# Kernel tuning notes

Measured on AMD Instinct MI355X. Metric: run time of the kernel, lower is better.

## Reference

```python
import jax, jax.numpy as jnp
import numpy as np


def _cubic(x):
    absx = np.abs(x)
    absx2 = absx ** 2
    absx3 = absx ** 3
    return ((1.5 * absx3 - 2.5 * absx2 + 1) * (absx <= 1)
            + (-0.5 * absx3 + 2.5 * absx2 - 4 * absx + 2) * ((1 < absx) & (absx <= 2)))


def _contributions(in_length, out_length, scale):
    # Replicates Resizer.contributions for cubic kernel with antialiasing (scale < 1).
    kernel_width = 4.0 / scale
    fixed_kernel = lambda arg: scale * _cubic(scale * arg)
    out_coordinates = np.arange(1, out_length + 1)
    shifted = out_coordinates - (out_length - in_length * scale) / 2
    match = shifted / scale + 0.5 * (1 - 1 / scale)
    left = np.floor(match - kernel_width / 2)
    expanded = int(np.ceil(kernel_width) + 2)
    fov = np.int16(left[:, None] + np.arange(expanded) - 1)  # (out, taps)
    weights = fixed_kernel(1.0 * match[:, None] - fov - 1)
    s = np.sum(weights, axis=1)
    s[s == 0] = 1.0
    weights = weights / s[:, None]
    mirror = np.concatenate((np.arange(in_length), np.arange(in_length - 1, -1, -1)))
    fov = mirror[np.mod(fov, mirror.shape[0])]
    nz = np.nonzero(np.any(weights, axis=0))[0]  # drop all-zero taps
    return weights[:, nz], fov[:, nz]


IN_SHAPE = (32, 3, 512, 512)
OUT_HW = 256
SCALE = 0.5
NDIM_TRAIL = 3  # len(scale_factor) - 1 trailing singleton dims on weights


def setup_inputs() -> dict:
    key = jax.random.key(0)
    in_tensor = jax.random.normal(key, IN_SHAPE, dtype=jnp.float32)
    w_np, fov_np = _contributions(IN_SHAPE[2], OUT_HW, SCALE)
    taps, out_len = w_np.shape[1], w_np.shape[0]
    w = jnp.asarray(w_np.T.reshape((taps, out_len) + (1,) * NDIM_TRAIL), dtype=jnp.float32)
    fov = jnp.asarray(fov_np.T, dtype=jnp.int32)  # (taps, out)
    # H and W have identical in/out lengths and scale -> identical tables
    return {"in_tensor": in_tensor, "w2": w, "fov2": fov, "w3": w, "fov3": fov}


def reference(in_tensor, w2, fov2, w3, fov3):
    x = in_tensor
    for dim, fov, w in ((2, fov2, w2), (3, fov3, w3)):
        x = jnp.swapaxes(x, dim, 0)          # bring resized axis to front
        x = jnp.sum(x[fov] * w, axis=0)      # gather (taps,out,...) * w -> (out,...)
        x = jnp.swapaxes(x, dim, 0)
    return x
```

## Files before the change

kernel.cpp:

```cpp
#include <hip/hip_runtime.h>


#define H_IN   512
#define W_IN   512
#define H_OUT  256
#define W_OUT  256
#define BC     96
#define TAPS   8
#define OH_T   8
#define OW_T   128
#define IN_ROWS (2 * OH_T + 6)
#define MID_COLS (2 * OW_T + 6)

__device__ __forceinline__ int mir(int r, int n) {
    r = (r < 0) ? (-1 - r) : r;
    r = (r >= n) ? (2 * n - 1 - r) : r;
    return r;
}

__global__ __launch_bounds__(256) void resize_fused(const float* __restrict__ in,
                                                    const float* __restrict__ wt,
                                                    float* __restrict__ out) {
    __shared__ float mid[OH_T][MID_COLS];

    const int bid = blockIdx.x;
    const int owt = bid & 1;
    const int oht = (bid >> 1) & 31;
    const int bc  = bid >> 6;
    const int oh0 = oht * OH_T;
    const int ow0 = owt * OW_T;
    const int t   = threadIdx.x;

    float K[TAPS];
#pragma unroll
    for (int i = 0; i < TAPS; ++i) K[i] = wt[i * H_OUT];

    const float* src = in + (size_t)bc * H_IN * W_IN;
    const int rbase = 2 * oh0 - 3;
    const int cbase = 2 * ow0 - 3;

    for (int c = t; c < MID_COLS; c += 256) {
        const int gc = mir(cbase + c, W_IN);
        float acc[OH_T];
#pragma unroll
        for (int k = 0; k < OH_T; ++k) acc[k] = 0.f;

#pragma unroll
        for (int r = 0; r < IN_ROWS; ++r) {
            const float x = src[(size_t)mir(rbase + r, H_IN) * W_IN + gc];
#pragma unroll
            for (int k = 0; k < OH_T; ++k) {
                const int i = r - 2 * k;
                if (0 <= i && i < TAPS) acc[k] += K[i] * x;
            }
        }
#pragma unroll
        for (int k = 0; k < OH_T; ++k) mid[k][c] = acc[k];
    }

    __syncthreads();

    const int owl = t & (OW_T - 1);
    const int r0  = (t >> 7) * 4;
    float* dst = out + ((size_t)bc * H_OUT + oh0) * W_OUT + ow0 + owl;

#pragma unroll
    for (int rr = 0; rr < 4; ++rr) {
        const int row = r0 + rr;
        float s = 0.f;
#pragma unroll
        for (int j = 0; j < TAPS; ++j)
            s += K[j] * mid[row][2 * owl + j];
        dst[(size_t)row * W_OUT] = s;
    }
}

extern "C" void kernel_launch(void* const* d_in, const int* in_sizes, int n_in,
                              void* d_out, int out_size, void* d_ws, size_t ws_size,
                              hipStream_t stream) {
    const float* in = (const float*)d_in[0];
    const float* w2 = (const float*)d_in[1];
    float* out = (float*)d_out;
    (void)d_ws; (void)ws_size;

    resize_fused<<<BC * 32 * 2, 256, 0, stream>>>(in, w2, out);
}
```

Baseline: 158.5 us.

## Process full-width row tiles with float4 loads and register-windowed horizontal pass

Each block now covers a full 512-column input strip for 8 output rows instead of splitting width into two tiles. This removes the duplicated halo columns and column mirroring in the vertical pass. The vertical pass uses float4 global loads per thread. The horizontal pass builds a 24-element register window from shared memory, computes 8 outputs per thread, and stores them as float4, handling mirroring only at the edge column groups. Blocks shrink to 128 threads and the grid is halved, which may reduce occupancy and latency hiding. The W-dimension weights are now read from their own input instead of reusing the H table.

```diff
diff --git a/kernel.cpp b/kernel.cpp
--- a/kernel.cpp
+++ b/kernel.cpp
@@ -8,9 +8,8 @@
 #define BC     96
 #define TAPS   8
 #define OH_T   8
-#define OW_T   128
 #define IN_ROWS (2 * OH_T + 6)
-#define MID_COLS (2 * OW_T + 6)
+#define MID_STRIDE 514
 
 __device__ __forceinline__ int mir(int r, int n) {
     r = (r < 0) ? (-1 - r) : r;
@@ -18,60 +17,90 @@
     return r;
 }
 
-__global__ __launch_bounds__(256) void resize_fused(const float* __restrict__ in,
-                                                    const float* __restrict__ wt,
+__global__ __launch_bounds__(128) void resize_fused(const float* __restrict__ in,
+                                                    const float* __restrict__ wh,
+                                                    const float* __restrict__ ww,
                                                     float* __restrict__ out) {
-    __shared__ float mid[OH_T][MID_COLS];
+    __shared__ float mid[OH_T * MID_STRIDE];
 
-    const int bid = blockIdx.x;
-    const int owt = bid & 1;
-    const int oht = (bid >> 1) & 31;
-    const int bc  = bid >> 6;
-    const int oh0 = oht * OH_T;
-    const int ow0 = owt * OW_T;
+    const int oht = blockIdx.x & 31;
+    const int bc  = blockIdx.x >> 5;
     const int t   = threadIdx.x;
 
-    float K[TAPS];
+    float KH[TAPS];
 #pragma unroll
-    for (int i = 0; i < TAPS; ++i) K[i] = wt[i * H_OUT];
+    for (int i = 0; i < TAPS; ++i) KH[i] = wh[i * H_OUT];
 
-    const float* src = in + (size_t)bc * H_IN * W_IN;
-    const int rbase = 2 * oh0 - 3;
-    const int cbase = 2 * ow0 - 3;
+    const float4* src = (const float4*)(in + (size_t)bc * H_IN * W_IN) + t;
+    const int rbase = 16 * oht - 3;
 
-    for (int c = t; c < MID_COLS; c += 256) {
-        const int gc = mir(cbase + c, W_IN);
-        float acc[OH_T];
+    float4 acc[OH_T];
 #pragma unroll
-        for (int k = 0; k < OH_T; ++k) acc[k] = 0.f;
+    for (int k = 0; k < OH_T; ++k) acc[k] = make_float4(0.f, 0.f, 0.f, 0.f);
 
 #pragma unroll
-        for (int r = 0; r < IN_ROWS; ++r) {
-            const float x = src[(size_t)mir(rbase + r, H_IN) * W_IN + gc];
+    for (int r = 0; r < IN_ROWS; ++r) {
+        const int rm = mir(rbase + r, H_IN);
+        const float4 x = src[(size_t)rm * (W_IN / 4)];
 #pragma unroll
-            for (int k = 0; k < OH_T; ++k) {
-                const int i = r - 2 * k;
-                if (0 <= i && i < TAPS) acc[k] += K[i] * x;
+        for (int k = 0; k < OH_T; ++k) {
+            const int i = r - 2 * k;
+            if (0 <= i && i < TAPS) {
+                const float kw = KH[i];
+                acc[k].x += kw * x.x;
+                acc[k].y += kw * x.y;
+                acc[k].z += kw * x.z;
+                acc[k].w += kw * x.w;
             }
         }
+    }
 #pragma unroll
-        for (int k = 0; k < OH_T; ++k) mid[k][c] = acc[k];
+    for (int k = 0; k < OH_T; ++k) {
+        float2* m2 = (float2*)&mid[k * MID_STRIDE + 4 * t];
+        m2[0] = make_float2(acc[k].x, acc[k].y);
+        m2[1] = make_float2(acc[k].z, acc[k].w);
     }
 
     __syncthreads();
 
-    const int owl = t & (OW_T - 1);
-    const int r0  = (t >> 7) * 4;
-    float* dst = out + ((size_t)bc * H_OUT + oh0) * W_OUT + ow0 + owl;
+    float KW[TAPS];
+#pragma unroll
+    for (int i = 0; i < TAPS; ++i) KW[i] = ww[i * W_OUT];
+
+    const int r   = t & 7;
+    const int cg0 = t >> 3;
+    const int oh  = 8 * oht + r;
+    float* drow = out + ((size_t)bc * H_OUT + oh) * W_OUT;
 
 #pragma unroll
-    for (int rr = 0; rr < 4; ++rr) {
-        const int row = r0 + rr;
-        float s = 0.f;
+    for (int cc = 0; cc < 2; ++cc) {
+        const int cg = cg0 + 16 * cc;
+        float win[24];
+        if (cg == 0 || cg == 31) {
 #pragma unroll
-        for (int j = 0; j < TAPS; ++j)
-            s += K[j] * mid[row][2 * owl + j];
-        dst[(size_t)row * W_OUT] = s;
+            for (int w = 0; w < 24; ++w)
+                win[w] = mid[r * MID_STRIDE + mir(16 * cg - 4 + w, W_IN)];
+        } else {
+            const float2* s2 = (const float2*)&mid[r * MID_STRIDE + 16 * cg - 4];
+#pragma unroll
+            for (int v = 0; v < 12; ++v) {
+                const float2 d = s2[v];
+                win[2 * v]     = d.x;
+                win[2 * v + 1] = d.y;
+            }
+        }
+        float res[8];
+#pragma unroll
+        for (int m = 0; m < 8; ++m) {
+            float s = 0.f;
+#pragma unroll
+            for (int j = 0; j < TAPS; ++j)
+                s += KW[j] * win[2 * m + j + 1];
+            res[m] = s;
+        }
+        float4* dv = (float4*)(drow + 8 * cg);
+        dv[0] = make_float4(res[0], res[1], res[2], res[3]);
+        dv[1] = make_float4(res[4], res[5], res[6], res[7]);
     }
 }
 
@@ -80,8 +109,9 @@
                               hipStream_t stream) {
     const float* in = (const float*)d_in[0];
     const float* w2 = (const float*)d_in[1];
+    const float* w3 = (const float*)d_in[3];
     float* out = (float*)d_out;
     (void)d_ws; (void)ws_size;
 
-    resize_fused<<<BC * 32 * 2, 256, 0, stream>>>(in, w2, out);
+    resize_fused<<<BC * 32, 128, 0, stream>>>(in, w2, w3, out);
 }
```

Result: no change. 160.2 us (+1.1%).
